# Kernel tuning notes

Hardware: AMD Instinct MI355X
Metric: run time of the kernel (lower is better)

The kernel has to match this reference:

```python
import jax, jax.numpy as jnp
import numpy as np


def setup_inputs() -> dict:
    key = jax.random.key(0)
    k1, k2 = jax.random.split(key)
    b, n, d = 8, 4096, 512
    num_codebooks, codebook_size = 1, 8192
    x = jax.random.normal(k1, (b, n, d), dtype=jnp.float32)
    embed = jax.random.normal(k2, (num_codebooks, codebook_size, d), dtype=jnp.float32)
    return {"x": x, "embed": embed}


def reference(x, embed):
    # Eval-mode forward of EuclideanCodebook (temperature 0 -> argmax of -cdist).
    # x: [b, n, d]; embed: [h, C, d] with h = num_codebooks = 1.
    b, n, d = x.shape
    h, C, _ = embed.shape
    flatten = x.reshape(h, b * n, d)                       # h * d packing (h=1)

    # dist = -cdist(flatten, embed): negative euclidean distance [h, N, C]
    x2 = jnp.sum(flatten * flatten, axis=-1, keepdims=True)   # [h, N, 1]
    e2 = jnp.sum(embed * embed, axis=-1)[:, None, :]          # [h, 1, C]
    xe = jnp.einsum('hnd,hcd->hnc', flatten, embed)           # [h, N, C]
    d2 = jnp.clip(x2 + e2 - 2.0 * xe, 0.0)
    dist = -jnp.sqrt(d2)                                      # [h, N, C]

    # gumbel_sample at temp 0 / eval -> straight argmax
    embed_ind_flat = jnp.argmax(dist, axis=-1)                # [h, N]

    # quantize = batched_embedding(embed_ind, embed): gather codes
    quantize = jnp.take_along_axis(embed, embed_ind_flat[..., None], axis=1)  # [h, N, d]

    # unpack + drop the codebook dim (needs_codebook_dim path)
    quantize = quantize.reshape(b, n, d)
    embed_ind = embed_ind_flat.reshape(b, n)
    dist = dist.reshape(h, b, n, C)  # dist keeps the codebook dim, as in source
    return quantize, embed_ind, dist
```

## Files before the change

### kernel.cpp

```cpp
#include <hip/hip_runtime.h>
#include <hip/hip_fp16.h>
#include <stdint.h>

typedef _Float16 f16x8 __attribute__((ext_vector_type(8)));
typedef _Float16 f16x4 __attribute__((ext_vector_type(4)));
typedef float    f32x4 __attribute__((ext_vector_type(4)));

static constexpr int NROWS = 32768;
static constexpr int NCODE = 8192;
static constexpr int DDIM  = 512;
static constexpr int BM = 256, BN = 256, BK = 64;
static constexpr int NBM = NROWS / BM;
static constexpr int NBN = NCODE / BN;
static constexpr int NPART = NBN * 2;

static constexpr size_t OFF_IND  = (size_t)NROWS * DDIM;
static constexpr size_t OFF_DIST = OFF_IND + NROWS;

static constexpr size_t WS_XH   = 0;
static constexpr size_t WS_XL   = WS_XH + (size_t)NROWS * DDIM * 2;
static constexpr size_t WS_EH   = WS_XL + (size_t)NROWS * DDIM * 2;
static constexpr size_t WS_EL   = WS_EH + (size_t)NCODE * DDIM * 2;
static constexpr size_t WS_X2   = WS_EL + (size_t)NCODE * DDIM * 2;
static constexpr size_t WS_E2   = WS_X2 + (size_t)NROWS * 4;
static constexpr size_t WS_PART = WS_E2 + (size_t)NCODE * 4;

__device__ inline void gload_lds16(const void* g, void* l) {
  __builtin_amdgcn_global_load_lds((const __attribute__((address_space(1))) void*)g,
                                   (__attribute__((address_space(3))) void*)l,
                                   16, 0, 0);
}

__global__ __launch_bounds__(128)
void prep_kernel(const float* __restrict__ x, const float* __restrict__ e,
                 _Float16* __restrict__ xh, _Float16* __restrict__ xl,
                 _Float16* __restrict__ eh, _Float16* __restrict__ el,
                 float* __restrict__ x2, float* __restrict__ e2)
{
  int bid = blockIdx.x;
  const float* src; _Float16 *dh, *dl; float* nrm;
  if (bid < NROWS) {
    src = x + (size_t)bid * DDIM;
    dh = xh + (size_t)bid * DDIM;  dl = xl + (size_t)bid * DDIM;
    nrm = x2 + bid;
  } else {
    int r = bid - NROWS;
    src = e + (size_t)r * DDIM;
    dh = eh + (size_t)r * DDIM;    dl = el + (size_t)r * DDIM;
    nrm = e2 + r;
  }
  int t = threadIdx.x;
  float4 v = reinterpret_cast<const float4*>(src)[t];
  double s = (double)v.x*v.x + (double)v.y*v.y + (double)v.z*v.z + (double)v.w*v.w;
  f16x4 h, l;
  h.x = (_Float16)v.x; l.x = (_Float16)(v.x - (float)h.x);
  h.y = (_Float16)v.y; l.y = (_Float16)(v.y - (float)h.y);
  h.z = (_Float16)v.z; l.z = (_Float16)(v.z - (float)h.z);
  h.w = (_Float16)v.w; l.w = (_Float16)(v.w - (float)h.w);
  reinterpret_cast<f16x4*>(dh)[t] = h;
  reinterpret_cast<f16x4*>(dl)[t] = l;
  #pragma unroll
  for (int m = 1; m < 64; m <<= 1) s += __shfl_xor(s, m);
  __shared__ double sh[2];
  if ((t & 63) == 0) sh[t >> 6] = s;
  __syncthreads();
  if (t == 0) nrm[0] = (float)(sh[0] + sh[1]);
}

__global__ __launch_bounds__(512, 1)
void dist_gemm_kernel(const _Float16* __restrict__ xh, const _Float16* __restrict__ xl,
                      const _Float16* __restrict__ eh, const _Float16* __restrict__ el,
                      const float* __restrict__ x2, const float* __restrict__ e2,
                      float* __restrict__ dist, float2* __restrict__ part)
{
  __shared__ _Float16 L[2][2][BM * BK];

  const int tid  = threadIdx.x;
  const int wid  = tid >> 6;
  const int lane = tid & 63;
  const int qwr  = wid >> 1;
  const int qwc  = wid & 1;

  const int flat = blockIdx.x;
  const int xcd  = flat & 7;
  const int idx  = flat >> 3;
  const int bn   = xcd * 4 + (idx & 3);
  const int bm   = idx >> 2;
  const int R  = bm * BM;
  const int Cc = bn * BN;

  const int l3 = lane >> 3;
  const int l7 = lane & 7;
  const int srcslot = ((l7 ^ l3) << 4);

  auto STAGE_HALF = [&](int t, int nb, int half) {
    const int ab = half & 1;
    const int hh = half >> 1;
    const _Float16* base;
    size_t rowbase;
    if (ab == 0) { base = (t < 16) ? xh : xl;              rowbase = (size_t)R;  }
    else         { base = (t < 8 || t >= 16) ? eh : el;    rowbase = (size_t)Cc; }
    const int k0b = (t & 7) * (BK * 2);
    #pragma unroll
    for (int i = 0; i < 2; ++i) {
      const int rr = hh * 128 + wid * 16 + i * 8;
      gload_lds16((const char*)base + (rowbase + rr + l3) * (DDIM * 2) + k0b + srcslot,
                  &L[nb][ab][rr * BK]);
    }
  };

  const int l15   = lane & 15;
  const int kslot = (lane >> 4) << 4;

  auto LDA = [&](f16x8 (&af)[2][2], int b, int mq) {
    #pragma unroll
    for (int m = 0; m < 2; ++m)
      #pragma unroll
      for (int ks = 0; ks < 2; ++ks) {
        const int row = mq * 128 + qwr * 32 + m * 16 + l15;
        const int kb  = (ks * 64 + kslot) ^ ((row & 7) << 4);
        af[m][ks] = *(const f16x8*)((const char*)&L[b][0][0] + row * 128 + kb);
      }
  };
  auto LDB = [&](f16x8 (&bf)[4][2], int b, int nq) {
    #pragma unroll
    for (int n = 0; n < 4; ++n)
      #pragma unroll
      for (int ks = 0; ks < 2; ++ks) {
        const int row = nq * 128 + qwc * 64 + n * 16 + l15;
        const int kb  = (ks * 64 + kslot) ^ ((row & 7) << 4);
        bf[n][ks] = *(const f16x8*)((const char*)&L[b][1][0] + row * 128 + kb);
      }
  };

  f32x4 acc[2][2][2][4] = {};

  auto MM = [&](f32x4 (&ac)[2][4], f16x8 (&af)[2][2], f16x8 (&bf)[4][2]) {
    #pragma unroll
    for (int m = 0; m < 2; ++m)
      #pragma unroll
      for (int n = 0; n < 4; ++n)
        #pragma unroll
        for (int ks = 0; ks < 2; ++ks)
          ac[m][n] = __builtin_amdgcn_mfma_f32_16x16x32_f16(af[m][ks], bf[n][ks], ac[m][n], 0, 0, 0);
  };

  STAGE_HALF(0, 0, 0);
  STAGE_HALF(0, 0, 1);
  STAGE_HALF(0, 0, 2);
  STAGE_HALF(0, 0, 3);

  for (int t = 0; t < 24; ++t) {
    const int b = t & 1;
    f16x8 af0[2][2], af1[2][2], bf0[4][2], bf1[4][2];

    if (t < 23) { STAGE_HALF(t + 1, b ^ 1, 0);
                  asm volatile("s_waitcnt vmcnt(6)" ::: "memory"); }
    else        { asm volatile("s_waitcnt vmcnt(4)" ::: "memory"); }
    __builtin_amdgcn_s_barrier();
    LDA(af0, b, 0);
    LDB(bf0, b, 0);
    __builtin_amdgcn_s_setprio(1);
    MM(acc[0][0], af0, bf0);
    __builtin_amdgcn_s_setprio(0);
    __builtin_amdgcn_s_barrier();

    if (t < 23) { STAGE_HALF(t + 1, b ^ 1, 1);
                  asm volatile("s_waitcnt vmcnt(6)" ::: "memory"); }
    else        { asm volatile("s_waitcnt vmcnt(2)" ::: "memory"); }
    __builtin_amdgcn_s_barrier();
    LDA(af1, b, 1);
    __builtin_amdgcn_s_setprio(1);
    MM(acc[1][0], af1, bf0);
    __builtin_amdgcn_s_setprio(0);
    __builtin_amdgcn_s_barrier();

    if (t < 23) { STAGE_HALF(t + 1, b ^ 1, 2);
                  asm volatile("s_waitcnt vmcnt(6)" ::: "memory"); }
    else        { asm volatile("s_waitcnt vmcnt(0)" ::: "memory"); }
    __builtin_amdgcn_s_barrier();
    LDB(bf1, b, 1);
    __builtin_amdgcn_s_setprio(1);
    MM(acc[1][1], af1, bf1);
    __builtin_amdgcn_s_setprio(0);
    __builtin_amdgcn_s_barrier();

    if (t < 23) STAGE_HALF(t + 1, b ^ 1, 3);
    __builtin_amdgcn_s_setprio(1);
    MM(acc[0][1], af0, bf1);
    __builtin_amdgcn_s_setprio(0);
    __builtin_amdgcn_s_barrier();
  }

  const int q    = lane >> 4;
  const int csub = lane & 15;

  float e2v[2][4];
  #pragma unroll
  for (int nq = 0; nq < 2; ++nq)
    #pragma unroll
    for (int n = 0; n < 4; ++n)
      e2v[nq][n] = e2[Cc + nq * 128 + qwc * 64 + n * 16 + csub];

  float bestv[16], besti[16];
  int rix = 0;
  #pragma unroll
  for (int mq = 0; mq < 2; ++mq)
    #pragma unroll
    for (int m = 0; m < 2; ++m)
      #pragma unroll
      for (int j = 0; j < 4; ++j, ++rix) {
        const int row = R + mq * 128 + qwr * 32 + m * 16 + q * 4 + j;
        const float xv = x2[row];
        float* drow = dist + (size_t)row * NCODE;
        float bv = -3.0e38f, bi = 0.0f;
        #pragma unroll
        for (int nq = 0; nq < 2; ++nq)
          #pragma unroll
          for (int n = 0; n < 4; ++n) {
            const int col = Cc + nq * 128 + qwc * 64 + n * 16 + csub;
            float xe = acc[mq][nq][m][n][j];
            float d2 = fmaxf((xv + e2v[nq][n]) - 2.0f * xe, 0.0f);
            float dv = -sqrtf(d2);
            drow[col] = dv;
            if (dv > bv) { bv = dv; bi = (float)col; }
          }
        bestv[rix] = bv;
        besti[rix] = bi;
      }

  #pragma unroll
  for (int msk = 1; msk < 16; msk <<= 1) {
    #pragma unroll
    for (int r = 0; r < 16; ++r) {
      float ov = __shfl_xor(bestv[r], msk);
      float oi = __shfl_xor(besti[r], msk);
      if (ov > bestv[r] || (ov == bestv[r] && oi < besti[r])) { bestv[r] = ov; besti[r] = oi; }
    }
  }
  if (csub == 0) {
    int rr = 0;
    #pragma unroll
    for (int mq = 0; mq < 2; ++mq)
      #pragma unroll
      for (int m = 0; m < 2; ++m)
        #pragma unroll
        for (int j = 0; j < 4; ++j, ++rr) {
          const int row = R + mq * 128 + qwr * 32 + m * 16 + q * 4 + j;
          part[(size_t)row * NPART + bn * 2 + qwc] = make_float2(bestv[rr], besti[rr]);
        }
  }
}

__global__ __launch_bounds__(64)
void reduce_gather_kernel(const float2* __restrict__ part, const float* __restrict__ embed,
                          float* __restrict__ quant, float* __restrict__ ind)
{
  const int row = blockIdx.x;
  const int l = threadIdx.x;
  float2 a = part[(size_t)row * NPART + l];
  float bv = a.x, bi = a.y;
  #pragma unroll
  for (int m = 1; m < 64; m <<= 1) {
    float ov = __shfl_xor(bv, m);
    float oi = __shfl_xor(bi, m);
    if (ov > bv || (ov == bv && oi < bi)) { bv = ov; bi = oi; }
  }
  if (l == 0) ind[row] = bi;
  const int idx = (int)bi;
  const float4* src = reinterpret_cast<const float4*>(embed + (size_t)idx * DDIM);
  float4* dst = reinterpret_cast<float4*>(quant + (size_t)row * DDIM);
  dst[l]      = src[l];
  dst[l + 64] = src[l + 64];
}

extern "C" void kernel_launch(void* const* d_in, const int* in_sizes, int n_in,
                              void* d_out, int out_size, void* d_ws, size_t ws_size,
                              hipStream_t stream) {
  const float* x     = (const float*)d_in[0];
  const float* embed = (const float*)d_in[1];

  char* ws = (char*)d_ws;
  _Float16* xh = (_Float16*)(ws + WS_XH);
  _Float16* xl = (_Float16*)(ws + WS_XL);
  _Float16* eh = (_Float16*)(ws + WS_EH);
  _Float16* el = (_Float16*)(ws + WS_EL);
  float*    x2 = (float*)(ws + WS_X2);
  float*    e2 = (float*)(ws + WS_E2);
  float2*   part = (float2*)(ws + WS_PART);

  float* quant = (float*)d_out;
  float* ind   = (float*)d_out + OFF_IND;
  float* dist  = (float*)d_out + OFF_DIST;

  prep_kernel<<<dim3(NROWS + NCODE), 128, 0, stream>>>(x, embed, xh, xl, eh, el, x2, e2);
  dist_gemm_kernel<<<dim3(NBM * NBN), 512, 0, stream>>>(xh, xl, eh, el, x2, e2, dist, part);
  reduce_gather_kernel<<<dim3(NROWS), 64, 0, stream>>>(part, embed, quant, ind);
}
```

Before: 998.8 us.

## Software-pipeline LDS fragment loads one phase ahead of MFMA work

Restructures the main GEMM loop so that LDS fragment loads for the next phase, including the first A/B fragments of the next tile, are issued before the current MFMA batch and overlap with it. The loop is unrolled by two with ping-pong register fragment sets. Barriers drop from two per phase to one, and the vmcnt waits are retuned. This aims to hide LDS read latency behind MFMA execution, at the cost of higher register pressure and a more delicate barrier and waitcnt ordering, where a mistake could cause a race on the double-buffered LDS.

```diff
diff --git a/kernel.cpp b/kernel.cpp
--- a/kernel.cpp
+++ b/kernel.cpp
@@ -136,6 +136,7 @@
   f32x4 acc[2][2][2][4] = {};
 
   auto MM = [&](f32x4 (&ac)[2][4], f16x8 (&af)[2][2], f16x8 (&bf)[4][2]) {
+    __builtin_amdgcn_s_setprio(1);
     #pragma unroll
     for (int m = 0; m < 2; ++m)
       #pragma unroll
@@ -143,53 +144,53 @@
         #pragma unroll
         for (int ks = 0; ks < 2; ++ks)
           ac[m][n] = __builtin_amdgcn_mfma_f32_16x16x32_f16(af[m][ks], bf[n][ks], ac[m][n], 0, 0, 0);
+    __builtin_amdgcn_s_setprio(0);
+  };
+
+  auto TILE = [&](int t, int b, f16x8 (&af0)[2][2], f16x8 (&bf0)[4][2],
+                  f16x8 (&af0n)[2][2], f16x8 (&bf0n)[4][2]) {
+    f16x8 af1[2][2], bf1[4][2];
+
+    if (t < 23) { STAGE_HALF(t + 1, b ^ 1, 0);
+                  LDA(af1, b, 1);
+                  asm volatile("s_waitcnt vmcnt(2)" ::: "memory"); }
+    else        { LDA(af1, b, 1);
+                  asm volatile("s_waitcnt vmcnt(0)" ::: "memory"); }
+    __builtin_amdgcn_s_barrier();
+    MM(acc[0][0], af0, bf0);
+
+    if (t < 23) STAGE_HALF(t + 1, b ^ 1, 1);
+    LDB(bf1, b, 1);
+    __builtin_amdgcn_s_barrier();
+    MM(acc[1][0], af1, bf0);
+
+    if (t < 23) { STAGE_HALF(t + 1, b ^ 1, 2);
+                  asm volatile("s_waitcnt vmcnt(2)" ::: "memory"); }
+    __builtin_amdgcn_s_barrier();
+    MM(acc[1][1], af1, bf1);
+
+    if (t < 23) { STAGE_HALF(t + 1, b ^ 1, 3);
+                  LDA(af0n, b ^ 1, 0);
+                  LDB(bf0n, b ^ 1, 0);
+                  asm volatile("s_waitcnt vmcnt(2)" ::: "memory"); }
+    __builtin_amdgcn_s_barrier();
+    MM(acc[0][1], af0, bf1);
   };
 
   STAGE_HALF(0, 0, 0);
   STAGE_HALF(0, 0, 1);
   STAGE_HALF(0, 0, 2);
   STAGE_HALF(0, 0, 3);
-
-  for (int t = 0; t < 24; ++t) {
-    const int b = t & 1;
-    f16x8 af0[2][2], af1[2][2], bf0[4][2], bf1[4][2];
-
-    if (t < 23) { STAGE_HALF(t + 1, b ^ 1, 0);
-                  asm volatile("s_waitcnt vmcnt(6)" ::: "memory"); }
-    else        { asm volatile("s_waitcnt vmcnt(4)" ::: "memory"); }
-    __builtin_amdgcn_s_barrier();
-    LDA(af0, b, 0);
-    LDB(bf0, b, 0);
-    __builtin_amdgcn_s_setprio(1);
-    MM(acc[0][0], af0, bf0);
-    __builtin_amdgcn_s_setprio(0);
-    __builtin_amdgcn_s_barrier();
-
-    if (t < 23) { STAGE_HALF(t + 1, b ^ 1, 1);
-                  asm volatile("s_waitcnt vmcnt(6)" ::: "memory"); }
-    else        { asm volatile("s_waitcnt vmcnt(2)" ::: "memory"); }
-    __builtin_amdgcn_s_barrier();
-    LDA(af1, b, 1);
-    __builtin_amdgcn_s_setprio(1);
-    MM(acc[1][0], af1, bf0);
-    __builtin_amdgcn_s_setprio(0);
-    __builtin_amdgcn_s_barrier();
-
-    if (t < 23) { STAGE_HALF(t + 1, b ^ 1, 2);
-                  asm volatile("s_waitcnt vmcnt(6)" ::: "memory"); }
-    else        { asm volatile("s_waitcnt vmcnt(0)" ::: "memory"); }
-    __builtin_amdgcn_s_barrier();
-    LDB(bf1, b, 1);
-    __builtin_amdgcn_s_setprio(1);
-    MM(acc[1][1], af1, bf1);
-    __builtin_amdgcn_s_setprio(0);
-    __builtin_amdgcn_s_barrier();
-
-    if (t < 23) STAGE_HALF(t + 1, b ^ 1, 3);
-    __builtin_amdgcn_s_setprio(1);
-    MM(acc[0][1], af0, bf1);
-    __builtin_amdgcn_s_setprio(0);
-    __builtin_amdgcn_s_barrier();
+  asm volatile("s_waitcnt vmcnt(2)" ::: "memory");
+  __builtin_amdgcn_s_barrier();
+
+  f16x8 afA[2][2], bfA[4][2], afB[2][2], bfB[4][2];
+  LDA(afA, 0, 0);
+  LDB(bfA, 0, 0);
+
+  for (int tt = 0; tt < 24; tt += 2) {
+    TILE(tt,     0, afA, bfA, afB, bfB);
+    TILE(tt + 1, 1, afB, bfB, afA, bfA);
   }
 
   const int q    = lane >> 4;
```

Result: slower. 3.052 ms (+205.6%).

## Restructure GEMM main loop into deeper software pipeline with peeled epilogue

Applied to the files above, without the earlier changes.

Reorders the K-loop so LDS fragment loads for the current quarter are issued before the next global-to-LDS stage and its barrier. Stage 0 of the tile two steps ahead is prefetched during the current iteration. The last two iterations are peeled into explicit epilogues with adjusted vmcnt waits. The aim is to overlap global loads, LDS reads and MFMA work more tightly and remove barrier stalls, at the cost of a more fragile wait-count and buffer-reuse schedule.

```diff
diff --git a/kernel.cpp b/kernel.cpp
--- a/kernel.cpp
+++ b/kernel.cpp
@@ -67,6 +67,22 @@
   if (t == 0) nrm[0] = (float)(sh[0] + sh[1]);
 }
 
+#define BARx __builtin_amdgcn_s_barrier()
+#define VMC(n)  asm volatile("s_waitcnt vmcnt(" #n ")" ::: "memory")
+
+__device__ __forceinline__ void MMX(f32x4 (&ac)[2][4], const f16x8 (&af)[2][2],
+                                    const f16x8 (&bf)[4][2]) {
+  __builtin_amdgcn_s_setprio(1);
+  #pragma unroll
+  for (int m = 0; m < 2; ++m)
+    #pragma unroll
+    for (int n = 0; n < 4; ++n)
+      #pragma unroll
+      for (int ks = 0; ks < 2; ++ks)
+        ac[m][n] = __builtin_amdgcn_mfma_f32_16x16x32_f16(af[m][ks], bf[n][ks], ac[m][n], 0, 0, 0);
+  __builtin_amdgcn_s_setprio(0);
+}
+
 __global__ __launch_bounds__(512, 1)
 void dist_gemm_kernel(const _Float16* __restrict__ xh, const _Float16* __restrict__ xl,
                       const _Float16* __restrict__ eh, const _Float16* __restrict__ el,
@@ -135,61 +151,67 @@
 
   f32x4 acc[2][2][2][4] = {};
 
-  auto MM = [&](f32x4 (&ac)[2][4], f16x8 (&af)[2][2], f16x8 (&bf)[4][2]) {
-    #pragma unroll
-    for (int m = 0; m < 2; ++m)
-      #pragma unroll
-      for (int n = 0; n < 4; ++n)
-        #pragma unroll
-        for (int ks = 0; ks < 2; ++ks)
-          ac[m][n] = __builtin_amdgcn_mfma_f32_16x16x32_f16(af[m][ks], bf[n][ks], ac[m][n], 0, 0, 0);
-  };
-
   STAGE_HALF(0, 0, 0);
   STAGE_HALF(0, 0, 1);
   STAGE_HALF(0, 0, 2);
   STAGE_HALF(0, 0, 3);
-
-  for (int t = 0; t < 24; ++t) {
+  STAGE_HALF(1, 1, 0);
+  VMC(6);
+  BARx;
+
+  for (int t = 0; t < 22; ++t) {
     const int b = t & 1;
     f16x8 af0[2][2], af1[2][2], bf0[4][2], bf1[4][2];
 
-    if (t < 23) { STAGE_HALF(t + 1, b ^ 1, 0);
-                  asm volatile("s_waitcnt vmcnt(6)" ::: "memory"); }
-    else        { asm volatile("s_waitcnt vmcnt(4)" ::: "memory"); }
-    __builtin_amdgcn_s_barrier();
-    LDA(af0, b, 0);
-    LDB(bf0, b, 0);
-    __builtin_amdgcn_s_setprio(1);
-    MM(acc[0][0], af0, bf0);
-    __builtin_amdgcn_s_setprio(0);
-    __builtin_amdgcn_s_barrier();
-
-    if (t < 23) { STAGE_HALF(t + 1, b ^ 1, 1);
-                  asm volatile("s_waitcnt vmcnt(6)" ::: "memory"); }
-    else        { asm volatile("s_waitcnt vmcnt(2)" ::: "memory"); }
-    __builtin_amdgcn_s_barrier();
+    LDA(af0, b, 0);  LDB(bf0, b, 0);
+    STAGE_HALF(t + 1, b ^ 1, 1);
+    VMC(6);  BARx;
+    MMX(acc[0][0], af0, bf0);
+
     LDA(af1, b, 1);
-    __builtin_amdgcn_s_setprio(1);
-    MM(acc[1][0], af1, bf0);
-    __builtin_amdgcn_s_setprio(0);
-    __builtin_amdgcn_s_barrier();
-
-    if (t < 23) { STAGE_HALF(t + 1, b ^ 1, 2);
-                  asm volatile("s_waitcnt vmcnt(6)" ::: "memory"); }
-    else        { asm volatile("s_waitcnt vmcnt(0)" ::: "memory"); }
-    __builtin_amdgcn_s_barrier();
+    STAGE_HALF(t + 1, b ^ 1, 2);
+    VMC(6);  BARx;
+    MMX(acc[1][0], af1, bf0);
+
     LDB(bf1, b, 1);
-    __builtin_amdgcn_s_setprio(1);
-    MM(acc[1][1], af1, bf1);
-    __builtin_amdgcn_s_setprio(0);
-    __builtin_amdgcn_s_barrier();
-
-    if (t < 23) STAGE_HALF(t + 1, b ^ 1, 3);
-    __builtin_amdgcn_s_setprio(1);
-    MM(acc[0][1], af0, bf1);
-    __builtin_amdgcn_s_setprio(0);
-    __builtin_amdgcn_s_barrier();
+    STAGE_HALF(t + 1, b ^ 1, 3);
+    BARx;
+    MMX(acc[1][1], af1, bf1);
+
+    STAGE_HALF(t + 2, b, 0);
+    VMC(6);  BARx;
+    MMX(acc[0][1], af0, bf1);
+  }
+
+  {
+    f16x8 af0[2][2], af1[2][2], bf0[4][2], bf1[4][2];
+    LDA(af0, 0, 0);  LDB(bf0, 0, 0);
+    STAGE_HALF(23, 1, 1);
+    VMC(6);  BARx;
+    MMX(acc[0][0], af0, bf0);
+    LDA(af1, 0, 1);
+    STAGE_HALF(23, 1, 2);
+    VMC(6);  BARx;
+    MMX(acc[1][0], af1, bf0);
+    LDB(bf1, 0, 1);
+    STAGE_HALF(23, 1, 3);
+    BARx;
+    MMX(acc[1][1], af1, bf1);
+    VMC(4);  BARx;
+    MMX(acc[0][1], af0, bf1);
+  }
+  {
+    f16x8 af0[2][2], af1[2][2], bf0[4][2], bf1[4][2];
+    LDA(af0, 1, 0);  LDB(bf0, 1, 0);
+    VMC(2);  BARx;
+    MMX(acc[0][0], af0, bf0);
+    LDA(af1, 1, 1);
+    VMC(0);  BARx;
+    MMX(acc[1][0], af1, bf0);
+    LDB(bf1, 1, 1);
+    BARx;
+    MMX(acc[1][1], af1, bf1);
+    MMX(acc[0][1], af0, bf1);
   }
 
   const int q    = lane >> 4;
```

New measurement: 945.5 us. 1.06x faster.
